# Kernel tuning notes

Hardware: AMD Instinct MI355X
Metric: run time of the kernel (lower is better)

## Reference

```python
import jax, jax.numpy as jnp
import numpy as np

N_NODES = 50000
N_EDGES = 800000
D_IN = 128
D_HID = 128
BN_EPS = 1e-5


def _sage_mean(h, src, dst, w_self, w_neigh, b):
    # DGL SAGEConv('mean'): out = h @ W_self + mean_{neighbors}(h_src) @ W_neigh + bias
    msg = h[src]                                               # [E, D] gather
    ssum = jax.ops.segment_sum(msg, dst, num_segments=N_NODES)  # [N, D]
    deg = jax.ops.segment_sum(jnp.ones((src.shape[0],), h.dtype), dst,
                              num_segments=N_NODES)            # [N]
    mean = ssum / jnp.maximum(deg, 1.0)[:, None]
    return h @ w_self + mean @ w_neigh + b


def _bn_relu(h, gamma, beta):
    # BatchNorm1d with batch statistics (training-mode math), then ReLU.
    m = jnp.mean(h, axis=0)
    v = jnp.mean(jnp.square(h - m), axis=0)  # biased variance, as torch uses for normalization
    hn = (h - m) * jax.lax.rsqrt(v + BN_EPS) * gamma + beta
    return jax.nn.relu(hn)


def setup_inputs() -> dict:
    key = jax.random.key(0)
    ks = jax.random.split(key, 16)
    x = jax.random.normal(ks[0], (N_NODES, D_IN), dtype=jnp.float32)
    src = jax.random.randint(ks[1], (N_EDGES,), 0, N_NODES, dtype=jnp.int32)
    dst = jax.random.randint(ks[2], (N_EDGES,), 0, N_NODES, dtype=jnp.int32)
    s0 = 1.0 / np.sqrt(D_IN)
    s1 = 1.0 / np.sqrt(D_HID)
    inp = {
        'x': x, 'src': src, 'dst': dst,
        'W_self0': jax.random.uniform(ks[3], (D_IN, D_HID), jnp.float32, -s0, s0),
        'W_neigh0': jax.random.uniform(ks[4], (D_IN, D_HID), jnp.float32, -s0, s0),
        'b0': jnp.zeros((D_HID,), jnp.float32),
        'W_self1': jax.random.uniform(ks[5], (D_HID, D_HID), jnp.float32, -s1, s1),
        'W_neigh1': jax.random.uniform(ks[6], (D_HID, D_HID), jnp.float32, -s1, s1),
        'b1': jnp.zeros((D_HID,), jnp.float32),
        'W_self2': jax.random.uniform(ks[7], (D_HID, D_HID), jnp.float32, -s1, s1),
        'W_neigh2': jax.random.uniform(ks[8], (D_HID, D_HID), jnp.float32, -s1, s1),
        'b2': jnp.zeros((D_HID,), jnp.float32),
        'gamma0': jnp.ones((D_HID,), jnp.float32),
        'beta0': jnp.zeros((D_HID,), jnp.float32),
        'gamma1': jnp.ones((D_HID,), jnp.float32),
        'beta1': jnp.zeros((D_HID,), jnp.float32),
    }
    return inp


def reference(x, src, dst,
              W_self0, W_neigh0, b0,
              W_self1, W_neigh1, b1,
              W_self2, W_neigh2, b2,
              gamma0, beta0, gamma1, beta1):
    h = _sage_mean(x, src, dst, W_self0, W_neigh0, b0)
    h = _bn_relu(h, gamma0, beta0)  # dropout is identity in eval mode
    h = _sage_mean(h, src, dst, W_self1, W_neigh1, b1)
    h = _bn_relu(h, gamma1, beta1)
    h = _sage_mean(h, src, dst, W_self2, W_neigh2, b2)
    return h
```

## Files before the change

### kernel.cpp

```cpp
#include <hip/hip_runtime.h>

#define N_NODES 50000
#define N_EDGES 800000
#define D 128
#define BN_EPS 1e-5f

#define NBUCK 391
#define BSHIFT 7
#define S1_BLOCKS 256
#define EPB 3125
#define CVT_BLOCKS 6250
#define PACK_BLOCKS 384

typedef __attribute__((ext_vector_type(8))) short bf16x8;
typedef __attribute__((ext_vector_type(4))) float f32x4;

__device__ inline unsigned short f2bf(float f) {
    unsigned int u = __float_as_uint(f);
    u = (u + 0x7FFF + ((u >> 16) & 1)) >> 16;
    return (unsigned short)u;
}

__device__ inline float bf2f(unsigned short b) {
    return __uint_as_float(((unsigned)b) << 16);
}

__device__ __forceinline__ void acc_plain(float* a, uint4 v) {
    unsigned w[4] = {v.x, v.y, v.z, v.w};
#pragma unroll
    for (int p = 0; p < 4; p++) {
        a[2 * p]     += __uint_as_float(w[p] << 16);
        a[2 * p + 1] += __uint_as_float(w[p] & 0xffff0000u);
    }
}

__device__ __forceinline__ void acc_bn(float* a, uint4 v, const float* sc, const float* sh) {
    unsigned w[4] = {v.x, v.y, v.z, v.w};
#pragma unroll
    for (int p = 0; p < 4; p++) {
        float lo = __uint_as_float(w[p] << 16);
        float hi = __uint_as_float(w[p] & 0xffff0000u);
        a[2 * p]     += fmaxf(lo * sc[2 * p]     + sh[2 * p],     0.f);
        a[2 * p + 1] += fmaxf(hi * sc[2 * p + 1] + sh[2 * p + 1], 0.f);
    }
}


__global__ void fused_prep(const float* __restrict__ x, unsigned short* __restrict__ x16,
                           const int* __restrict__ dst, int* __restrict__ hist,
                           const float* __restrict__ Ws0, const float* __restrict__ Wn0,
                           const float* __restrict__ Ws1, const float* __restrict__ Wn1,
                           const float* __restrict__ Ws2, const float* __restrict__ Wn2,
                           unsigned short* __restrict__ Wf, float* __restrict__ statsg) {
    __shared__ int lh[NBUCK];
    const int bid = blockIdx.x, t = threadIdx.x;

    if (bid < CVT_BLOCKS) {
        int idx = bid * 256 + t;
        float4 v = ((const float4*)x)[idx];
        ushort4 o;
        o.x = f2bf(v.x); o.y = f2bf(v.y); o.z = f2bf(v.z); o.w = f2bf(v.w);
        ((ushort4*)x16)[idx] = o;
    } else if (bid < CVT_BLOCKS + S1_BLOCKS) {
        int blk = bid - CVT_BLOCKS;
        for (int i = t; i < NBUCK; i += 256) lh[i] = 0;
        __syncthreads();
        int e0 = blk * EPB;
        for (int i = 0; i < 13; i++) {
            int k = t + i * 256;
            if (k < EPB) atomicAdd(&lh[dst[e0 + k] >> BSHIFT], 1);
        }
        __syncthreads();
        for (int i = t; i < NBUCK; i += 256) hist[blk * NBUCK + i] = lh[i];
    } else {
        if (bid == CVT_BLOCKS + S1_BLOCKS) {
            statsg[t] = 0.f; statsg[t + 256] = 0.f;
        }
        int idx = (bid - (CVT_BLOCKS + S1_BLOCKS)) * 256 + t;
        if (idx < 3 * 32768) {
            int layer = idx >> 15;
            int rem = idx & 32767;
            int kt = rem >> 12;
            int nt = (rem >> 9) & 7;
            int lane = (rem >> 3) & 63;
            int j = rem & 7;
            int k = kt * 32 + (lane >> 4) * 8 + j;
            int n = nt * 16 + (lane & 15);
            const float* Wsrc;
            if (layer == 0) Wsrc = (k < 128) ? Ws0 : Wn0;
            else if (layer == 1) Wsrc = (k < 128) ? Ws1 : Wn1;
            else Wsrc = (k < 128) ? Ws2 : Wn2;
            Wf[idx] = f2bf(Wsrc[(k & 127) * D + n]);
        }
    }
}


__global__ void s2a(int* __restrict__ hist, int* __restrict__ bucketTotal) {
    __shared__ int s[S1_BLOCKS];
    int b = blockIdx.x, t = threadIdx.x;
    int v = hist[t * NBUCK + b];
    s[t] = v;
    __syncthreads();
    for (int off = 1; off < S1_BLOCKS; off <<= 1) {
        int x = (t >= off) ? s[t - off] : 0;
        __syncthreads();
        s[t] += x;
        __syncthreads();
    }
    hist[t * NBUCK + b] = s[t] - v;
    if (t == S1_BLOCKS - 1) bucketTotal[b] = s[t];
}


__global__ void s3_scatter(const int* __restrict__ src, const int* __restrict__ dst,
                           const int* __restrict__ hist, const int* __restrict__ bucketTotal,
                           int* __restrict__ bucketStart, unsigned int* __restrict__ rec) {
    __shared__ int sc[512];
    __shared__ int base[NBUCK];
    int blk = blockIdx.x, t = threadIdx.x;
    int i1 = t + 256;
    int v0 = (t < NBUCK) ? bucketTotal[t] : 0;
    int v1 = (i1 < NBUCK) ? bucketTotal[i1] : 0;
    sc[t] = v0; sc[i1] = v1;
    __syncthreads();
    for (int off = 1; off < 512; off <<= 1) {
        int x0 = (t >= off) ? sc[t - off] : 0;
        int x1 = (i1 >= off) ? sc[i1 - off] : 0;
        __syncthreads();
        sc[t] += x0; sc[i1] += x1;
        __syncthreads();
    }
    if (t < NBUCK)  base[t]  = (sc[t] - v0)  + hist[blk * NBUCK + t];
    if (i1 < NBUCK) base[i1] = (sc[i1] - v1) + hist[blk * NBUCK + i1];
    if (blk == 0) {
        if (t < NBUCK)  bucketStart[t]  = sc[t] - v0;
        if (i1 < NBUCK) bucketStart[i1] = sc[i1] - v1;
        if (t == 0) bucketStart[NBUCK] = N_EDGES;
    }
    __syncthreads();
    int e0 = blk * EPB;
    for (int i = 0; i < 13; i++) {
        int k = t + i * 256;
        if (k < EPB) {
            int e = e0 + k;
            int d = dst[e];
            int p = atomicAdd(&base[d >> BSHIFT], 1);
            rec[p] = ((unsigned)(d & 127) << 16) | (unsigned)src[e];
        }
    }
}


__global__ void s4_build(const unsigned int* __restrict__ rec, const int* __restrict__ bucketStart,
                         unsigned short* __restrict__ csr, int* __restrict__ degi,
                         int* __restrict__ offsets, float* __restrict__ inv_deg) {
    __shared__ int lh[128];
    __shared__ int ls[128];
    __shared__ int lcur[128];
    int b = blockIdx.x, t = threadIdx.x;
    int start = bucketStart[b], end = bucketStart[b + 1];

    if (t < 128) lh[t] = 0;
    __syncthreads();
    for (int e = start + t; e < end; e += 256)
        atomicAdd(&lh[rec[e] >> 16], 1);
    __syncthreads();

    int v = 0;
    if (t < 128) { v = lh[t]; ls[t] = v; }
    __syncthreads();
    for (int off = 1; off < 128; off <<= 1) {
        int x = 0;
        if (t < 128 && t >= off) x = ls[t - off];
        __syncthreads();
        if (t < 128) ls[t] += x;
        __syncthreads();
    }

    int node0 = b << BSHIFT;
    if (t < 128) {
        int excl = ls[t] - v;
        lcur[t] = start + excl;
        int node = node0 + t;
        if (node < N_NODES) {
            degi[node] = v;
            offsets[node] = start + excl;
            inv_deg[node] = 1.0f / (float)max(v, 1);
        }
    }
    __syncthreads();
    for (int e = start + t; e < end; e += 256) {
        unsigned r = rec[e];
        int p = atomicAdd(&lcur[r >> 16], 1);
        csr[p] = (unsigned short)(r & 0xFFFFu);
    }
}


#define GATHER(k) (*(const uint4*)(h16 + (size_t)csr[beg + (k)] * D + c * 8))

__global__ void aggregate16(const unsigned short* __restrict__ h16,
                            const unsigned short* __restrict__ csr, const int* __restrict__ offsets,
                            const int* __restrict__ degi, const float* __restrict__ inv_deg,
                            unsigned short* __restrict__ mean16,
                            const float* __restrict__ statsIn,
                            const float* __restrict__ gammaIn, const float* __restrict__ betaIn) {
    int node = blockIdx.x * 16 + (threadIdx.x >> 4);
    if (node >= N_NODES) return;
    int c = threadIdx.x & 15;
    int beg = offsets[node], n = degi[node];
    float a[8];
#pragma unroll
    for (int j = 0; j < 8; j++) a[j] = 0.f;

    if (statsIn) {
        const float invN = 1.0f / (float)N_NODES;
        float sc[8], sh[8];
#pragma unroll
        for (int j = 0; j < 8; j++) {
            int col = c * 8 + j;
            float m = statsIn[col] * invN;
            float var = statsIn[128 + col] * invN - m * m;
            float s = rsqrtf(var + BN_EPS) * gammaIn[col];
            sc[j] = s;
            sh[j] = betaIn[col] - m * s;
        }
        int i = 0;
        if (n >= 4) {
            uint4 v0 = GATHER(0), v1 = GATHER(1), v2 = GATHER(2), v3 = GATHER(3);
            for (i = 4; i + 3 < n; i += 4) {
                uint4 w0 = GATHER(i), w1 = GATHER(i + 1), w2 = GATHER(i + 2), w3 = GATHER(i + 3);
                acc_bn(a, v0, sc, sh); acc_bn(a, v1, sc, sh);
                acc_bn(a, v2, sc, sh); acc_bn(a, v3, sc, sh);
                v0 = w0; v1 = w1; v2 = w2; v3 = w3;
            }
            acc_bn(a, v0, sc, sh); acc_bn(a, v1, sc, sh);
            acc_bn(a, v2, sc, sh); acc_bn(a, v3, sc, sh);
        }
        for (; i < n; i++) { uint4 v = GATHER(i); acc_bn(a, v, sc, sh); }
    } else {
        int i = 0;
        if (n >= 4) {
            uint4 v0 = GATHER(0), v1 = GATHER(1), v2 = GATHER(2), v3 = GATHER(3);
            for (i = 4; i + 3 < n; i += 4) {
                uint4 w0 = GATHER(i), w1 = GATHER(i + 1), w2 = GATHER(i + 2), w3 = GATHER(i + 3);
                acc_plain(a, v0); acc_plain(a, v1); acc_plain(a, v2); acc_plain(a, v3);
                v0 = w0; v1 = w1; v2 = w2; v3 = w3;
            }
            acc_plain(a, v0); acc_plain(a, v1); acc_plain(a, v2); acc_plain(a, v3);
        }
        for (; i < n; i++) { uint4 v = GATHER(i); acc_plain(a, v); }
    }

    float w = inv_deg[node];
    uint4 o;
    o.x = ((unsigned)f2bf(a[1] * w) << 16) | f2bf(a[0] * w);
    o.y = ((unsigned)f2bf(a[3] * w) << 16) | f2bf(a[2] * w);
    o.z = ((unsigned)f2bf(a[5] * w) << 16) | f2bf(a[4] * w);
    o.w = ((unsigned)f2bf(a[7] * w) << 16) | f2bf(a[6] * w);
    *(uint4*)(mean16 + (size_t)node * D + c * 8) = o;
}


__global__ __launch_bounds__(256) void sage_gemm(
    const unsigned short* __restrict__ h16, const unsigned short* __restrict__ mean16,
    const unsigned short* __restrict__ Wf, const float* __restrict__ bias,
    unsigned short* __restrict__ out16, float* __restrict__ outf,
    float* __restrict__ statsOut,
    const float* __restrict__ statsIn,
    const float* __restrict__ gammaIn, const float* __restrict__ betaIn) {
    __shared__ float sstat[256];
    const int t = threadIdx.x;
    const int lane = t & 63;
    const int wave = t >> 6;
    const int m = lane & 15;
    const int quad = lane >> 4;
    const int wrow0 = blockIdx.x * 64 + wave * 16;
    const float invN = 1.0f / (float)N_NODES;

    if (statsOut) {
        sstat[t] = 0.f;
        __syncthreads();
    }

    int arow = wrow0 + m;
    if (arow >= N_NODES) arow = N_NODES - 1;

    f32x4 acc[8];
#pragma unroll
    for (int i = 0; i < 8; i++) acc[i] = (f32x4)(0.f);

#pragma unroll
    for (int kt = 0; kt < 8; kt++) {
        bf16x8 af;
        if (kt < 4) {
            af = *(const bf16x8*)(h16 + (size_t)arow * D + kt * 32 + quad * 8);
            if (statsIn) {
                int c0 = kt * 32 + quad * 8;
#pragma unroll
                for (int j = 0; j < 8; j++) {
                    int col = c0 + j;
                    float mm = statsIn[col] * invN;
                    float var = statsIn[128 + col] * invN - mm * mm;
                    float s = rsqrtf(var + BN_EPS) * gammaIn[col];
                    float raw = bf2f((unsigned short)af[j]);
                    float v = fmaxf(raw * s + (betaIn[col] - mm * s), 0.f);
                    af[j] = (short)f2bf(v);
                }
            }
        } else {
            af = *(const bf16x8*)(mean16 + (size_t)arow * D + (kt - 4) * 32 + quad * 8);
        }
#pragma unroll
        for (int nt = 0; nt < 8; nt++) {
            bf16x8 bf = *(const bf16x8*)(Wf + ((kt * 8 + nt) * 64 + lane) * 8);
            acc[nt] = __builtin_amdgcn_mfma_f32_16x16x32_bf16(af, bf, acc[nt], 0, 0, 0);
        }
    }

    const bool do16 = (out16 != nullptr);
#pragma unroll
    for (int nt = 0; nt < 8; nt++) {
        int cidx = nt * 16 + m;
        float bv = bias[cidx];
        float s = 0.f, q = 0.f;
#pragma unroll
        for (int reg = 0; reg < 4; reg++) {
            int r = wrow0 + quad * 4 + reg;
            float v = acc[nt][reg] + bv;
            if (r < N_NODES) {
                if (do16) out16[(size_t)r * D + cidx] = f2bf(v);
                else      outf[(size_t)r * D + cidx] = v;
                s += v; q += v * v;
            }
        }
        if (statsOut) {
            s += __shfl_xor(s, 16); s += __shfl_xor(s, 32);
            q += __shfl_xor(q, 16); q += __shfl_xor(q, 32);
            if (quad == 0) {
                atomicAdd(&sstat[cidx], s);
                atomicAdd(&sstat[128 + cidx], q);
            }
        }
    }
    if (statsOut) {
        __syncthreads();
        atomicAdd(&statsOut[t], sstat[t]);
    }
}


extern "C" void kernel_launch(void* const* d_in, const int* in_sizes, int n_in,
                              void* d_out, int out_size, void* d_ws, size_t ws_size,
                              hipStream_t stream) {
    const float* x   = (const float*)d_in[0];
    const int* src   = (const int*)d_in[1];
    const int* dst   = (const int*)d_in[2];
    const float* Ws0 = (const float*)d_in[3];
    const float* Wn0 = (const float*)d_in[4];
    const float* b0  = (const float*)d_in[5];
    const float* Ws1 = (const float*)d_in[6];
    const float* Wn1 = (const float*)d_in[7];
    const float* b1  = (const float*)d_in[8];
    const float* Ws2 = (const float*)d_in[9];
    const float* Wn2 = (const float*)d_in[10];
    const float* b2  = (const float*)d_in[11];
    const float* g0  = (const float*)d_in[12];
    const float* be0 = (const float*)d_in[13];
    const float* g1  = (const float*)d_in[14];
    const float* be1 = (const float*)d_in[15];

    char* base = (char*)d_ws;
    size_t NND = (size_t)N_NODES * D;
    unsigned short* X16    = (unsigned short*)base;
    unsigned short* H16    = (unsigned short*)(base + NND * 2);
    unsigned short* mean16 = (unsigned short*)(base + 2 * NND * 2);
    char* p = base + 6 * NND;
    unsigned short* Wf = (unsigned short*)p;  p += 3 * 32768 * 2;
    int* hist          = (int*)p;             p += (size_t)S1_BLOCKS * NBUCK * 4;
    int* bucketTotal   = (int*)p;             p += 1568;
    int* bucketStart   = (int*)p;             p += 1600;
    unsigned int* rec  = (unsigned int*)p;    p += (size_t)N_EDGES * 4;
    unsigned short* csr = (unsigned short*)p; p += (size_t)N_EDGES * 2;
    int* degi    = (int*)p;                   p += N_NODES * 4;
    int* offsets = (int*)p;                   p += N_NODES * 4;
    float* inv_deg = (float*)p;               p += N_NODES * 4;
    float* stats   = (float*)p;               p += 2048;
    float* stats0 = stats, *stats1 = stats + 256;

    fused_prep<<<CVT_BLOCKS + S1_BLOCKS + PACK_BLOCKS, 256, 0, stream>>>(
        x, X16, dst, hist, Ws0, Wn0, Ws1, Wn1, Ws2, Wn2, Wf, stats);
    s2a<<<NBUCK, 256, 0, stream>>>(hist, bucketTotal);
    s3_scatter<<<S1_BLOCKS, 256, 0, stream>>>(src, dst, hist, bucketTotal, bucketStart, rec);
    s4_build<<<NBUCK, 256, 0, stream>>>(rec, bucketStart, csr, degi, offsets, inv_deg);

    const int AGG_B = (N_NODES + 15) / 16;
    const int GEMM_B = (N_NODES + 63) / 64;

    aggregate16<<<AGG_B, 256, 0, stream>>>(X16, csr, offsets, degi, inv_deg, mean16,
                                           nullptr, nullptr, nullptr);
    sage_gemm<<<GEMM_B, 256, 0, stream>>>(X16, mean16, Wf, b0, H16, nullptr,
                                          stats0, nullptr, nullptr, nullptr);

    aggregate16<<<AGG_B, 256, 0, stream>>>(H16, csr, offsets, degi, inv_deg, mean16,
                                           stats0, g0, be0);
    sage_gemm<<<GEMM_B, 256, 0, stream>>>(H16, mean16, Wf + 32768, b1, X16, nullptr,
                                          stats1, stats0, g0, be0);

    aggregate16<<<AGG_B, 256, 0, stream>>>(X16, csr, offsets, degi, inv_deg, mean16,
                                           stats1, g1, be1);
    sage_gemm<<<GEMM_B, 256, 0, stream>>>(X16, mean16, Wf + 65536, b2, nullptr,
                                          (float*)d_out, nullptr, stats1, g1, be1);
}
```

Baseline: 331.3 us.

## Stage GEMM weights in LDS, replicate BN stats atomics, precompute BN scale/shift

The GEMM kernel now stages the packed bf16 weights into shared memory in two halves, and preloads all A fragments into registers before the MFMA loops, instead of having every wave read weights straight from global memory. BatchNorm statistics are accumulated into 8 replicated slots chosen by block index to spread global atomic contention. The first aggregate block folds those replicas into a precomputed scale/shift array that the following GEMM reads, which removes the per-element rsqrt work there. This adds LDS use (32KB per block) and extra barriers, with launch bounds that request 4 blocks per CU.

```diff
diff --git a/kernel.cpp b/kernel.cpp
--- a/kernel.cpp
+++ b/kernel.cpp
@@ -11,6 +11,7 @@
 #define EPB 3125
 #define CVT_BLOCKS 6250
 #define PACK_BLOCKS 384
+#define NREP 8
 
 typedef __attribute__((ext_vector_type(8))) short bf16x8;
 typedef __attribute__((ext_vector_type(4))) float f32x4;
@@ -74,7 +75,7 @@
         for (int i = t; i < NBUCK; i += 256) hist[blk * NBUCK + i] = lh[i];
     } else {
         if (bid == CVT_BLOCKS + S1_BLOCKS) {
-            statsg[t] = 0.f; statsg[t + 256] = 0.f;
+            for (int i = t; i < 2 * NREP * 256; i += 256) statsg[i] = 0.f;
         }
         int idx = (bid - (CVT_BLOCKS + S1_BLOCKS)) * 256 + t;
         if (idx < 3 * 32768) {
@@ -205,10 +206,27 @@
                             const int* __restrict__ degi, const float* __restrict__ inv_deg,
                             unsigned short* __restrict__ mean16,
                             const float* __restrict__ statsIn,
-                            const float* __restrict__ gammaIn, const float* __restrict__ betaIn) {
-    int node = blockIdx.x * 16 + (threadIdx.x >> 4);
+                            const float* __restrict__ gammaIn, const float* __restrict__ betaIn,
+                            float* __restrict__ scshG) {
+    int t = threadIdx.x;
+    if (statsIn && blockIdx.x == 0 && t < 128) {
+        const float invN = 1.0f / (float)N_NODES;
+        float s = 0.f, q = 0.f;
+#pragma unroll
+        for (int r = 0; r < NREP; r++) {
+            s += statsIn[r * 256 + t];
+            q += statsIn[r * 256 + 128 + t];
+        }
+        float m = s * invN;
+        float var = q * invN - m * m;
+        float scv = rsqrtf(var + BN_EPS) * gammaIn[t];
+        scshG[t] = scv;
+        scshG[128 + t] = betaIn[t] - m * scv;
+    }
+
+    int node = blockIdx.x * 16 + (t >> 4);
     if (node >= N_NODES) return;
-    int c = threadIdx.x & 15;
+    int c = t & 15;
     int beg = offsets[node], n = degi[node];
     float a[8];
 #pragma unroll
@@ -220,11 +238,17 @@
 #pragma unroll
         for (int j = 0; j < 8; j++) {
             int col = c * 8 + j;
-            float m = statsIn[col] * invN;
-            float var = statsIn[128 + col] * invN - m * m;
-            float s = rsqrtf(var + BN_EPS) * gammaIn[col];
-            sc[j] = s;
-            sh[j] = betaIn[col] - m * s;
+            float s = 0.f, q = 0.f;
+#pragma unroll
+            for (int r = 0; r < NREP; r++) {
+                s += statsIn[r * 256 + col];
+                q += statsIn[r * 256 + 128 + col];
+            }
+            float m = s * invN;
+            float var = q * invN - m * m;
+            float scv = rsqrtf(var + BN_EPS) * gammaIn[col];
+            sc[j] = scv;
+            sh[j] = betaIn[col] - m * scv;
         }
         int i = 0;
         if (n >= 4) {
@@ -263,59 +287,79 @@
 }
 
 
-__global__ __launch_bounds__(256) void sage_gemm(
+__global__ __launch_bounds__(256, 4) void sage_gemm(
     const unsigned short* __restrict__ h16, const unsigned short* __restrict__ mean16,
     const unsigned short* __restrict__ Wf, const float* __restrict__ bias,
     unsigned short* __restrict__ out16, float* __restrict__ outf,
-    float* __restrict__ statsOut,
-    const float* __restrict__ statsIn,
-    const float* __restrict__ gammaIn, const float* __restrict__ betaIn) {
+    float* __restrict__ statsOut, const float* __restrict__ scshG) {
+    __shared__ unsigned short sWf[16384];
     __shared__ float sstat[256];
     const int t = threadIdx.x;
     const int lane = t & 63;
-    const int wave = t >> 6;
     const int m = lane & 15;
     const int quad = lane >> 4;
-    const int wrow0 = blockIdx.x * 64 + wave * 16;
-    const float invN = 1.0f / (float)N_NODES;
-
-    if (statsOut) {
-        sstat[t] = 0.f;
-        __syncthreads();
-    }
+    const int wrow0 = blockIdx.x * 64 + (t >> 6) * 16;
 
     int arow = wrow0 + m;
     if (arow >= N_NODES) arow = N_NODES - 1;
 
+    bf16x8 afr[8];
+#pragma unroll
+    for (int kt = 0; kt < 4; kt++)
+        afr[kt] = *(const bf16x8*)(h16 + (size_t)arow * D + kt * 32 + quad * 8);
+#pragma unroll
+    for (int kt = 0; kt < 4; kt++)
+        afr[4 + kt] = *(const bf16x8*)(mean16 + (size_t)arow * D + kt * 32 + quad * 8);
+
+    const uint4* W4 = (const uint4*)Wf;
+    uint4* S4 = (uint4*)sWf;
+#pragma unroll
+    for (int i = 0; i < 8; i++) S4[i * 256 + t] = W4[i * 256 + t];
+    if (statsOut) sstat[t] = 0.f;
+    __syncthreads();
+
+    if (scshG) {
+#pragma unroll
+        for (int kt = 0; kt < 4; kt++) {
+            int c0 = kt * 32 + quad * 8;
+            float4 sca = *(const float4*)(scshG + c0);
+            float4 scb = *(const float4*)(scshG + c0 + 4);
+            float4 sha = *(const float4*)(scshG + 128 + c0);
+            float4 shb = *(const float4*)(scshG + 128 + c0 + 4);
+            float scv[8] = {sca.x, sca.y, sca.z, sca.w, scb.x, scb.y, scb.z, scb.w};
+            float shv[8] = {sha.x, sha.y, sha.z, sha.w, shb.x, shb.y, shb.z, shb.w};
+#pragma unroll
+            for (int j = 0; j < 8; j++) {
+                float v = fmaxf(bf2f((unsigned short)afr[kt][j]) * scv[j] + shv[j], 0.f);
+                afr[kt][j] = (short)f2bf(v);
+            }
+        }
+    }
+
     f32x4 acc[8];
 #pragma unroll
     for (int i = 0; i < 8; i++) acc[i] = (f32x4)(0.f);
 
 #pragma unroll
-    for (int kt = 0; kt < 8; kt++) {
-        bf16x8 af;
-        if (kt < 4) {
-            af = *(const bf16x8*)(h16 + (size_t)arow * D + kt * 32 + quad * 8);
-            if (statsIn) {
-                int c0 = kt * 32 + quad * 8;
-#pragma unroll
-                for (int j = 0; j < 8; j++) {
-                    int col = c0 + j;
-                    float mm = statsIn[col] * invN;
-                    float var = statsIn[128 + col] * invN - mm * mm;
-                    float s = rsqrtf(var + BN_EPS) * gammaIn[col];
-                    float raw = bf2f((unsigned short)af[j]);
-                    float v = fmaxf(raw * s + (betaIn[col] - mm * s), 0.f);
-                    af[j] = (short)f2bf(v);
-                }
-            }
-        } else {
-            af = *(const bf16x8*)(mean16 + (size_t)arow * D + (kt - 4) * 32 + quad * 8);
-        }
+    for (int kt = 0; kt < 4; kt++) {
 #pragma unroll
         for (int nt = 0; nt < 8; nt++) {
-            bf16x8 bf = *(const bf16x8*)(Wf + ((kt * 8 + nt) * 64 + lane) * 8);
-            acc[nt] = __builtin_amdgcn_mfma_f32_16x16x32_bf16(af, bf, acc[nt], 0, 0, 0);
+            bf16x8 bf = *(const bf16x8*)(sWf + ((kt * 8 + nt) * 64 + lane) * 8);
+            acc[nt] = __builtin_amdgcn_mfma_f32_16x16x32_bf16(afr[kt], bf, acc[nt], 0, 0, 0);
+        }
+    }
+
+    __syncthreads();
+#pragma unroll
+    for (int i = 0; i < 8; i++) S4[i * 256 + t] = W4[2048 + i * 256 + t];
+    __syncthreads();
+
+#pragma unroll
+    for (int kt = 4; kt < 8; kt++) {
+#pragma unroll
+        for (int nt = 0; nt < 8; nt++) {
+            bf16x8 bf = *(const bf16x8*)(sWf + (((kt - 4) * 8 + nt) * 64 + lane) * 8);
+            acc[nt] = __builtin_amdgcn_mfma_f32_16x16x32_bf16(afr[kt], bf, acc[nt], 0, 0, 0);
         }
     }
 
@@ -346,7 +390,7 @@
     }
     if (statsOut) {
         __syncthreads();
-        atomicAdd(&statsOut[t], sstat[t]);
+        atomicAdd(&statsOut[(blockIdx.x & (NREP - 1)) * 256 + t], sstat[t]);
     }
 }
 
@@ -386,8 +430,9 @@
     int* degi    = (int*)p;                   p += N_NODES * 4;
     int* offsets = (int*)p;                   p += N_NODES * 4;
     float* inv_deg = (float*)p;               p += N_NODES * 4;
-    float* stats   = (float*)p;               p += 2048;
-    float* stats0 = stats, *stats1 = stats + 256;
+    float* stats   = (float*)p;               p += 2 * NREP * 256 * 4;
+    float* scsh    = (float*)p;               p += 1024;
+    float* stats0 = stats, *stats1 = stats + NREP * 256;
 
     fused_prep<<<CVT_BLOCKS + S1_BLOCKS + PACK_BLOCKS, 256, 0, stream>>>(
         x, X16, dst, hist, Ws0, Wn0, Ws1, Wn1, Ws2, Wn2, Wf, stats);
@@ -399,17 +444,17 @@
     const int GEMM_B = (N_NODES + 63) / 64;
 
     aggregate16<<<AGG_B, 256, 0, stream>>>(X16, csr, offsets, degi, inv_deg, mean16,
-                                           nullptr, nullptr, nullptr);
+                                           nullptr, nullptr, nullptr, nullptr);
     sage_gemm<<<GEMM_B, 256, 0, stream>>>(X16, mean16, Wf, b0, H16, nullptr,
-                                          stats0, nullptr, nullptr, nullptr);
+                                          stats0, nullptr);
 
     aggregate16<<<AGG_B, 256, 0, stream>>>(H16, csr, offsets, degi, inv_deg, mean16,
-                                           stats0, g0, be0);
+                                           stats0, g0, be0, scsh);
     sage_gemm<<<GEMM_B, 256, 0, stream>>>(H16, mean16, Wf + 32768, b1, X16, nullptr,
-                                          stats1, stats0, g0, be0);
+                                          stats1, scsh);
 
     aggregate16<<<AGG_B, 256, 0, stream>>>(X16, csr, offsets, degi, inv_deg, mean16,
-                                           stats1, g1, be1);
+                                           stats1, g1, be1, scsh);
     sage_gemm<<<GEMM_B, 256, 0, stream>>>(X16, mean16, Wf + 65536, b2, nullptr,
-                                          (float*)d_out, nullptr, stats1, g1, be1);
-}
+                                          (float*)d_out, nullptr, scsh);
+}
```

Measured after the change: 317.5 us. 1.04x faster.
